# Performance work log

Hardware: AMD Instinct MI355X
Metric: run time of the kernel (lower is better)

## Reference

```python
import jax, jax.numpy as jnp
import numpy as np

MARGIN = 0.3
NEG_INF = jnp.float32(-1e30)


def setup_inputs() -> dict:
    key = jax.random.key(0)
    k1, k2 = jax.random.split(key)
    features = jax.random.normal(k1, (8192, 128), dtype=jnp.float32)
    labels = jax.random.randint(k2, (8192,), 0, 512)
    return {"features": features, "labels": labels}


def reference(features, labels):
    n = features.shape[0]
    # pairwise Euclidean distance, clamped like the torch code
    x2 = jnp.sum(features * features, axis=1, keepdims=True)          # [N,1]
    d2 = x2 + x2.T - 2.0 * (features @ features.T)                    # [N,N]
    dist = jnp.sqrt(jnp.clip(d2, 1e-8))

    same = labels[None, :] == labels[:, None]                          # [N,N]
    eye = jnp.eye(n, dtype=bool)
    pos_mask = same & ~eye                                             # positives, self excluded
    neg_mask = ~same

    # soft mining: softmax-weighted positive distance (weights ~ softmax(d))
    pos_logits = jnp.where(pos_mask, dist, NEG_INF)
    pw = jax.nn.softmax(pos_logits, axis=1)
    wp = jnp.sum(pw * jnp.where(pos_mask, dist, 0.0), axis=1)          # [N]

    # softmax-weighted negative distance (weights ~ softmax(-d))
    neg_logits = jnp.where(neg_mask, -dist, NEG_INF)
    nw = jax.nn.softmax(neg_logits, axis=1)
    wn = jnp.sum(nw * jnp.where(neg_mask, dist, 0.0), axis=1)          # [N]

    # soft margin: softplus(diff + margin)
    loss = jax.nn.softplus(wp - wn + MARGIN)

    # rows without any positive or any negative are skipped in the original
    valid = pos_mask.any(axis=1) & neg_mask.any(axis=1)
    loss = jnp.where(valid, loss, 0.0)
    denom = jnp.maximum(jnp.sum(valid.astype(jnp.float32)), 1.0)
    return jnp.sum(loss) / denom
```

## Files before the change

kernel.cpp:

```cpp
#include <hip/hip_runtime.h>
#include <hip/hip_bf16.h>


typedef __bf16 bf16x8 __attribute__((ext_vector_type(8)));
typedef float f32x4 __attribute__((ext_vector_type(4)));

#define NROWS 8192
#define DIM 128
#define JTILE 32
#define LDS_STRIDE 136
#define NLABELS 512
#define GCAP 64
#define JSPLIT 16
#define JSPAN (NROWS / JSPLIT)
#define JITERS (JSPAN / JTILE)
#define MARGIN_F 0.3f
#define AK1F 2.04027892f
#define AK1SQ 4.16273807f
#define EPS_T 2.08137e-8f
#define C2F (-43.2808512f)
#define LN2F 0.69314718f

__global__ __launch_bounds__(256) void prep_kernel(const float* __restrict__ F,
                                                   __hip_bfloat16* __restrict__ Fb,
                                                   float* __restrict__ x2,
                                                   float* __restrict__ gstat) {
    const int tid = threadIdx.x;
    const int wave = tid >> 6, lane = tid & 63;
    const int row = blockIdx.x * 4 + wave;
    float2 f = ((const float2*)(F + (size_t)row * DIM))[lane];
    f.x *= AK1F; f.y *= AK1F;
    ((__hip_bfloat162*)(Fb + (size_t)row * DIM))[lane] = __float22bfloat162_rn(f);
    float ss = f.x * f.x + f.y * f.y;
#pragma unroll
    for (int m = 32; m > 0; m >>= 1) ss += __shfl_xor(ss, m, 64);
    if (lane == 0) x2[row] = ss;
    if (blockIdx.x == 0 && tid < 4) gstat[tid] = 0.f;
}

template<bool DIAG>
__device__ __forceinline__ void tile_body(const __hip_bfloat16* __restrict__ sB,
                                          const float* __restrict__ sX2h,
                                          const bf16x8 (&a)[4],
                                          const float (&x2ih)[4],
                                          float (&nl4)[4], float (&ns4)[4],
                                          int lm, int quad, int ig0, int jbase) {
#pragma unroll
    for (int jt = 0; jt < 2; ++jt) {
        const int jl = jt * 16 + lm;
        const __hip_bfloat16* bp = sB + jl * LDS_STRIDE + quad * 8;
        const float xjh = sX2h[jl];
        f32x4 acc;
#pragma unroll
        for (int r = 0; r < 4; ++r) acc[r] = x2ih[r] + xjh;
#pragma unroll
        for (int kc = 0; kc < 4; ++kc) {
            bf16x8 b = *(const bf16x8*)(bp + kc * 32);
            acc = __builtin_amdgcn_mfma_f32_16x16x32_bf16(a[kc], b, acc, 0, 0, 0);
        }
        const int dj = jbase + jl - ig0;
#pragma unroll
        for (int r = 0; r < 4; ++r) {
            float d2h = fmaxf(-acc[r], EPS_T);
            float t = __builtin_amdgcn_sqrtf(d2h);
            float ne = __builtin_amdgcn_exp2f(-t);
            if (DIAG) ne = (dj == r) ? 0.f : ne;
            nl4[r] += ne;
            ns4[r] = fmaf(ne, t, ns4[r]);
        }
    }
}

__global__ __launch_bounds__(256, 3) void pairs_kernel(
        const __hip_bfloat16* __restrict__ Fb,
        const float* __restrict__ x2,
        const float* __restrict__ F,
        const int* __restrict__ labels,
        float2* __restrict__ partial,
        float4* __restrict__ corr) {
    __shared__ __hip_bfloat16 sB[2][JTILE * LDS_STRIDE];
    __shared__ float sX2[2][JTILE];
    __shared__ int sIdx[GCAP];
    __shared__ int sCnt;

    const int tid = threadIdx.x;
    const int bx = blockIdx.x, by = blockIdx.y;

    if (by < 4) {
        const int L = by * 128 + bx;
        if (tid == 0) sCnt = 0;
        __syncthreads();
        for (int it = 0; it < NROWS / 1024; ++it) {
            const int g = it * 1024 + tid * 4;
            int4 lv = *(const int4*)(labels + g);
#pragma unroll
            for (int k = 0; k < 4; ++k) {
                int lab = (k == 0) ? lv.x : (k == 1) ? lv.y : (k == 2) ? lv.z : lv.w;
                if (lab == L) {
                    int pos = atomicAdd(&sCnt, 1);
                    if (pos < GCAP) sIdx[pos] = g + k;
                }
            }
        }
        __syncthreads();
        const int gsz = sCnt < GCAP ? sCnt : GCAP;
        if (gsz > 0) {
            float* sAcc = (float*)sB;
            float* plA = sAcc;
            float* psA = sAcc + GCAP;
            float* nlA = sAcc + 2 * GCAP;
            float* nsA = sAcc + 3 * GCAP;
            if (tid < GCAP) { plA[tid] = 0.f; psA[tid] = 0.f; nlA[tid] = 0.f; nsA[tid] = 0.f; }
            __syncthreads();
            const int npair = gsz * gsz;
            for (int p = tid; p < npair; p += 256) {
                const int aI = p / gsz, bI = p - aI * gsz;
                if (aI == bI) continue;
                const float4* pa = (const float4*)(F + (size_t)sIdx[aI] * DIM);
                const float4* pb = (const float4*)(F + (size_t)sIdx[bI] * DIM);
                float dot = 0.f, ssa = 0.f, ssb = 0.f;
#pragma unroll 8
                for (int u = 0; u < 32; ++u) {
                    float4 va = pa[u], vb = pb[u];
                    dot = fmaf(va.x, vb.x, fmaf(va.y, vb.y, fmaf(va.z, vb.z, fmaf(va.w, vb.w, dot))));
                    ssa = fmaf(va.x, va.x, fmaf(va.y, va.y, fmaf(va.z, va.z, fmaf(va.w, va.w, ssa))));
                    ssb = fmaf(vb.x, vb.x, fmaf(vb.y, vb.y, fmaf(vb.z, vb.z, fmaf(vb.w, vb.w, ssb))));
                }
                float d2h = fmaxf((0.5f * (ssa + ssb) - dot) * AK1SQ, EPS_T);
                float t = __builtin_amdgcn_sqrtf(d2h);
                float ne = __builtin_amdgcn_exp2f(-t);
                float pe = __builtin_amdgcn_exp2f(t + C2F);
                unsafeAtomicAdd(&nlA[aI], ne);
                unsafeAtomicAdd(&nsA[aI], ne * t);
                unsafeAtomicAdd(&plA[aI], pe);
                unsafeAtomicAdd(&psA[aI], pe * t);
            }
            __syncthreads();
            if (tid < gsz)
                corr[sIdx[tid]] = make_float4(plA[tid], psA[tid], -nlA[tid], -nsA[tid]);
        }
        __syncthreads();
    }

    const int wave = tid >> 6;
    const int lane = tid & 63;
    const int quad = lane >> 4;
    const int lm = lane & 15;
    const int rbase = bx * 64 + wave * 16;

    bf16x8 a[4];
#pragma unroll
    for (int kc = 0; kc < 4; ++kc)
        a[kc] = *(const bf16x8*)(Fb + (size_t)(rbase + lm) * DIM + kc * 32 + quad * 8);

    const int ig0 = rbase + quad * 4;
    float x2ih[4];
#pragma unroll
    for (int r = 0; r < 4; ++r) x2ih[r] = -0.5f * x2[ig0 + r];

    float nl4[4] = {0,0,0,0}, ns4[4] = {0,0,0,0};

    const int j0 = by * JSPAN;
    const int djb0 = 2 * bx - by * JITERS;

    const int c0 = tid, c1 = tid + 256;
    uint4 st0, st1;
    float xv;
#define LOADTILE(JB) do {                                                      \
        const size_t jo = (size_t)(JB);                                        \
        st0 = *(const uint4*)(Fb + (jo + (c0 >> 4)) * DIM + (c0 & 15) * 8);    \
        st1 = *(const uint4*)(Fb + (jo + (c1 >> 4)) * DIM + (c1 & 15) * 8);    \
        if (tid < JTILE) xv = x2[jo + tid];                                    \
    } while (0)
#define WRITETILE(B) do {                                                      \
        __hip_bfloat16* sb = sB[B];                                            \
        *(uint4*)(sb + (c0 >> 4) * LDS_STRIDE + (c0 & 15) * 8) = st0;          \
        *(uint4*)(sb + (c1 >> 4) * LDS_STRIDE + (c1 & 15) * 8) = st1;          \
        if (tid < JTILE) sX2[B][tid] = -0.5f * xv;                             \
    } while (0)

    LOADTILE(j0);
    WRITETILE(0);
    __syncthreads();
    int cur = 0;
    for (int jb = 0; jb < JITERS; ++jb) {
        if (jb + 1 < JITERS) LOADTILE(j0 + (jb + 1) * JTILE);
        const int jbase = j0 + jb * JTILE;
        if ((unsigned)(jb - djb0) <= 1u)
            tile_body<true >(sB[cur], sX2[cur], a, x2ih, nl4, ns4, lm, quad, ig0, jbase);
        else
            tile_body<false>(sB[cur], sX2[cur], a, x2ih, nl4, ns4, lm, quad, ig0, jbase);
        if (jb + 1 < JITERS) WRITETILE(cur ^ 1);
        __syncthreads();
        cur ^= 1;
    }
#undef LOADTILE
#undef WRITETILE

#pragma unroll
    for (int m = 1; m < 16; m <<= 1) {
#pragma unroll
        for (int r = 0; r < 4; ++r) {
            nl4[r] += __shfl_xor(nl4[r], m, 64);
            ns4[r] += __shfl_xor(ns4[r], m, 64);
        }
    }
    if (lm == 0) {
#pragma unroll
        for (int r = 0; r < 4; ++r)
            partial[(size_t)by * NROWS + ig0 + r] = make_float2(nl4[r], ns4[r]);
    }
}

__global__ __launch_bounds__(256) void finalize_kernel(const float2* __restrict__ partial,
                                                       const float4* __restrict__ corr,
                                                       float* __restrict__ gstat,
                                                       float* __restrict__ out) {
    const int row = blockIdx.x * 256 + threadIdx.x;
    float4 c = corr[row];
    float nl = c.z, ns = c.w;
#pragma unroll
    for (int s = 0; s < JSPLIT; ++s) {
        float2 p = partial[(size_t)s * NROWS + row];
        nl += p.x; ns += p.y;
    }
    float sum = 0.f, cnt = 0.f;
    if (c.x > 0.f && nl > 0.f) {
        float x = fmaf(LN2F, c.y / c.x - ns / nl, MARGIN_F);
        sum = fmaxf(x, 0.f) + log1pf(__expf(-fabsf(x)));
        cnt = 1.f;
    }
#pragma unroll
    for (int m = 32; m > 0; m >>= 1) {
        sum += __shfl_xor(sum, m, 64);
        cnt += __shfl_xor(cnt, m, 64);
    }
    __shared__ float sS[4], sC[4];
    const int wave = threadIdx.x >> 6, lane = threadIdx.x & 63;
    if (lane == 0) { sS[wave] = sum; sC[wave] = cnt; }
    __syncthreads();
    if (threadIdx.x == 0) {
        unsafeAtomicAdd(&gstat[0], sS[0] + sS[1] + sS[2] + sS[3]);
        unsafeAtomicAdd(&gstat[1], sC[0] + sC[1] + sC[2] + sC[3]);
        __threadfence();
        unsigned t = atomicAdd((unsigned*)(gstat + 2), 1u);
        if (t == (unsigned)(gridDim.x - 1)) {
            float s2 = unsafeAtomicAdd(&gstat[0], 0.f);
            float c2 = unsafeAtomicAdd(&gstat[1], 0.f);
            out[0] = s2 / fmaxf(c2, 1.f);
        }
    }
}

extern "C" void kernel_launch(void* const* d_in, const int* in_sizes, int n_in,
                              void* d_out, int out_size, void* d_ws, size_t ws_size,
                              hipStream_t stream) {
    const float* F = (const float*)d_in[0];
    const int* labels = (const int*)d_in[1];
    float* out = (float*)d_out;

    char* ws = (char*)d_ws;
    __hip_bfloat16* Fb = (__hip_bfloat16*)ws;
    size_t off = (size_t)NROWS * DIM * 2;
    float* x2 = (float*)(ws + off);    off += (size_t)NROWS * 4;
    float4* corr = (float4*)(ws + off); off += (size_t)NROWS * 16;
    float2* partial = (float2*)(ws + off);
    off += (size_t)JSPLIT * NROWS * 8;
    float* gstat = (float*)(ws + off);

    prep_kernel<<<NROWS / 4, 256, 0, stream>>>(F, Fb, x2, gstat);
    pairs_kernel<<<dim3(NROWS / 64, JSPLIT), 256, 0, stream>>>(
        Fb, x2, F, labels, partial, corr);
    finalize_kernel<<<NROWS / 256, 256, 0, stream>>>(partial, corr, gstat, out);
}
```

Before: 109.7 us.

## Exploit distance symmetry: compute upper-triangle tiles and scatter column sums atomically

```diff
diff --git a/kernel.cpp b/kernel.cpp
--- a/kernel.cpp
+++ b/kernel.cpp
@@ -7,13 +7,12 @@
 
 #define NROWS 8192
 #define DIM 128
-#define JTILE 32
 #define LDS_STRIDE 136
 #define NLABELS 512
 #define GCAP 64
-#define JSPLIT 16
-#define JSPAN (NROWS / JSPLIT)
-#define JITERS (JSPAN / JTILE)
+#define NPAIR 64
+#define NCHUNK 32
+#define MTILES 129
 #define MARGIN_F 0.3f
 #define AK1F 2.04027892f
 #define AK1SQ 4.16273807f
@@ -44,9 +43,10 @@
                                           const bf16x8 (&a)[4],
                                           const float (&x2ih)[4],
                                           float (&nl4)[4], float (&ns4)[4],
+                                          float2* __restrict__ sColW,
                                           int lm, int quad, int ig0, int jbase) {
 #pragma unroll
-    for (int jt = 0; jt < 2; ++jt) {
+    for (int jt = 0; jt < 4; ++jt) {
         const int jl = jt * 16 + lm;
         const __hip_bfloat16* bp = sB + jl * LDS_STRIDE + quad * 8;
         const float xjh = sX2h[jl];
@@ -59,6 +59,7 @@
             acc = __builtin_amdgcn_mfma_f32_16x16x32_bf16(a[kc], b, acc, 0, 0, 0);
         }
         const int dj = jbase + jl - ig0;
+        float cl = 0.f, cs = 0.f;
 #pragma unroll
         for (int r = 0; r < 4; ++r) {
             float d2h = fmaxf(-acc[r], EPS_T);
@@ -67,6 +68,12 @@
             if (DIAG) ne = (dj == r) ? 0.f : ne;
             nl4[r] += ne;
             ns4[r] = fmaf(ne, t, ns4[r]);
+            if (!DIAG) { cl += ne; cs = fmaf(ne, t, cs); }
+        }
+        if (!DIAG) {
+            cl += __shfl_xor(cl, 16, 64); cl += __shfl_xor(cl, 32, 64);
+            cs += __shfl_xor(cs, 16, 64); cs += __shfl_xor(cs, 32, 64);
+            if (quad == 0) sColW[jl] = make_float2(cl, cs);
         }
     }
 }
@@ -76,18 +83,20 @@
         const float* __restrict__ x2,
         const float* __restrict__ F,
         const int* __restrict__ labels,
-        float2* __restrict__ partial,
+        float* __restrict__ accg,
         float4* __restrict__ corr) {
-    __shared__ __hip_bfloat16 sB[2][JTILE * LDS_STRIDE];
-    __shared__ float sX2[2][JTILE];
+    __shared__ __hip_bfloat16 sB[64 * LDS_STRIDE];
+    __shared__ float sX2[64];
+    __shared__ float2 sCol[4][64];
     __shared__ int sIdx[GCAP];
     __shared__ int sCnt;
 
     const int tid = threadIdx.x;
-    const int bx = blockIdx.x, by = blockIdx.y;
-
-    if (by < 4) {
-        const int L = by * 128 + bx;
+    const int p = blockIdx.x;
+    const int s = blockIdx.y;
+
+    if (s < 8) {
+        const int L = s * 64 + p;
         if (tid == 0) sCnt = 0;
         __syncthreads();
         for (int it = 0; it < NROWS / 1024; ++it) {
@@ -113,8 +122,8 @@
             if (tid < GCAP) { plA[tid] = 0.f; psA[tid] = 0.f; nlA[tid] = 0.f; nsA[tid] = 0.f; }
             __syncthreads();
             const int npair = gsz * gsz;
-            for (int p = tid; p < npair; p += 256) {
-                const int aI = p / gsz, bI = p - aI * gsz;
+            for (int pp = tid; pp < npair; pp += 256) {
+                const int aI = pp / gsz, bI = pp - aI * gsz;
                 if (aI == bI) continue;
                 const float4* pa = (const float4*)(F + (size_t)sIdx[aI] * DIM);
                 const float4* pb = (const float4*)(F + (size_t)sIdx[bI] * DIM);
@@ -146,84 +155,98 @@
     const int lane = tid & 63;
     const int quad = lane >> 4;
     const int lm = lane & 15;
-    const int rbase = bx * 64 + wave * 16;
-
-    bf16x8 a[4];
-#pragma unroll
-    for (int kc = 0; kc < 4; ++kc)
-        a[kc] = *(const bf16x8*)(Fb + (size_t)(rbase + lm) * DIM + kc * 32 + quad * 8);
-
-    const int ig0 = rbase + quad * 4;
-    float x2ih[4];
-#pragma unroll
-    for (int r = 0; r < 4; ++r) x2ih[r] = -0.5f * x2[ig0 + r];
-
-    float nl4[4] = {0,0,0,0}, ns4[4] = {0,0,0,0};
-
-    const int j0 = by * JSPAN;
-    const int djb0 = 2 * bx - by * JITERS;
-
-    const int c0 = tid, c1 = tid + 256;
-    uint4 st0, st1;
-    float xv;
-#define LOADTILE(JB) do {                                                      \
-        const size_t jo = (size_t)(JB);                                        \
-        st0 = *(const uint4*)(Fb + (jo + (c0 >> 4)) * DIM + (c0 & 15) * 8);    \
-        st1 = *(const uint4*)(Fb + (jo + (c1 >> 4)) * DIM + (c1 & 15) * 8);    \
-        if (tid < JTILE) xv = x2[jo + tid];                                    \
-    } while (0)
-#define WRITETILE(B) do {                                                      \
-        __hip_bfloat16* sb = sB[B];                                            \
-        *(uint4*)(sb + (c0 >> 4) * LDS_STRIDE + (c0 & 15) * 8) = st0;          \
-        *(uint4*)(sb + (c1 >> 4) * LDS_STRIDE + (c1 & 15) * 8) = st1;          \
-        if (tid < JTILE) sX2[B][tid] = -0.5f * xv;                             \
-    } while (0)
-
-    LOADTILE(j0);
-    WRITETILE(0);
-    __syncthreads();
-    int cur = 0;
-    for (int jb = 0; jb < JITERS; ++jb) {
-        if (jb + 1 < JITERS) LOADTILE(j0 + (jb + 1) * JTILE);
-        const int jbase = j0 + jb * JTILE;
-        if ((unsigned)(jb - djb0) <= 1u)
-            tile_body<true >(sB[cur], sX2[cur], a, x2ih, nl4, ns4, lm, quad, ig0, jbase);
-        else
-            tile_body<false>(sB[cur], sX2[cur], a, x2ih, nl4, ns4, lm, quad, ig0, jbase);
-        if (jb + 1 < JITERS) WRITETILE(cur ^ 1);
-        __syncthreads();
-        cur ^= 1;
-    }
-#undef LOADTILE
-#undef WRITETILE
-
-#pragma unroll
-    for (int m = 1; m < 16; m <<= 1) {
-#pragma unroll
-        for (int r = 0; r < 4; ++r) {
-            nl4[r] += __shfl_xor(nl4[r], m, 64);
-            ns4[r] += __shfl_xor(ns4[r], m, 64);
-        }
-    }
-    if (lm == 0) {
-#pragma unroll
-        for (int r = 0; r < 4; ++r)
-            partial[(size_t)by * NROWS + ig0 + r] = make_float2(nl4[r], ns4[r]);
-    }
-}
-
-__global__ __launch_bounds__(256) void finalize_kernel(const float2* __restrict__ partial,
+
+    const int nA = 128 - p;
+    const int tlo = (s * MTILES) >> 5;
+    const int thi = ((s + 1) * MTILES) >> 5;
+
+#pragma unroll 1
+    for (int phase = 0; phase < 2; ++phase) {
+        const int a = (phase == 0) ? p : 127 - p;
+        const int t0 = (phase == 0) ? tlo : (tlo > nA ? tlo : nA);
+        const int t1 = (phase == 0) ? (thi < nA ? thi : nA) : thi;
+        if (t0 >= t1) continue;
+
+        const int rbase = a * 64 + wave * 16;
+        bf16x8 afr[4];
+#pragma unroll
+        for (int kc = 0; kc < 4; ++kc)
+            afr[kc] = *(const bf16x8*)(Fb + (size_t)(rbase + lm) * DIM + kc * 32 + quad * 8);
+        const int ig0 = rbase + quad * 4;
+        float x2ih[4];
+#pragma unroll
+        for (int r = 0; r < 4; ++r) x2ih[r] = -0.5f * x2[ig0 + r];
+        float nl4[4] = {0,0,0,0}, ns4[4] = {0,0,0,0};
+
+        int prevj = -1;
+        for (int t = t0; t < t1; ++t) {
+            const int jb = (phase == 0) ? (p + t) : (127 - p) + (t - nA);
+            const int jbase = jb << 6;
+            __syncthreads();
+            if (prevj >= 0 && tid < 64) {
+                float2 c0 = sCol[0][tid], c1 = sCol[1][tid];
+                float2 c2 = sCol[2][tid], c3 = sCol[3][tid];
+                unsafeAtomicAdd(accg + (size_t)(prevj + tid) * 2,
+                                c0.x + c1.x + c2.x + c3.x);
+                unsafeAtomicAdd(accg + (size_t)(prevj + tid) * 2 + 1,
+                                c0.y + c1.y + c2.y + c3.y);
+            }
+#pragma unroll
+            for (int s2 = 0; s2 < 4; ++s2) {
+                int c = tid + s2 * 256;
+                int jr = c >> 4, ck = c & 15;
+                *(bf16x8*)(sB + jr * LDS_STRIDE + ck * 8) =
+                    *(const bf16x8*)(Fb + (size_t)(jbase + jr) * DIM + ck * 8);
+            }
+            if (tid < 64) sX2[tid] = -0.5f * x2[jbase + tid];
+            __syncthreads();
+
+            if (jb == a) {
+                tile_body<true >(sB, sX2, afr, x2ih, nl4, ns4, sCol[wave],
+                                 lm, quad, ig0, jbase);
+                prevj = -1;
+            } else {
+                tile_body<false>(sB, sX2, afr, x2ih, nl4, ns4, sCol[wave],
+                                 lm, quad, ig0, jbase);
+                prevj = jbase;
+            }
+        }
+
+#pragma unroll
+        for (int m = 1; m < 16; m <<= 1) {
+#pragma unroll
+            for (int r = 0; r < 4; ++r) {
+                nl4[r] += __shfl_xor(nl4[r], m, 64);
+                ns4[r] += __shfl_xor(ns4[r], m, 64);
+            }
+        }
+        if (lm == 0) {
+#pragma unroll
+            for (int r = 0; r < 4; ++r) {
+                unsafeAtomicAdd(accg + (size_t)(ig0 + r) * 2, nl4[r]);
+                unsafeAtomicAdd(accg + (size_t)(ig0 + r) * 2 + 1, ns4[r]);
+            }
+        }
+        __syncthreads();
+        if (prevj >= 0 && tid < 64) {
+            float2 c0 = sCol[0][tid], c1 = sCol[1][tid];
+            float2 c2 = sCol[2][tid], c3 = sCol[3][tid];
+            unsafeAtomicAdd(accg + (size_t)(prevj + tid) * 2,
+                            c0.x + c1.x + c2.x + c3.x);
+            unsafeAtomicAdd(accg + (size_t)(prevj + tid) * 2 + 1,
+                            c0.y + c1.y + c2.y + c3.y);
+        }
+    }
+}
+
+__global__ __launch_bounds__(256) void finalize_kernel(const float* __restrict__ accg,
                                                        const float4* __restrict__ corr,
                                                        float* __restrict__ gstat,
                                                        float* __restrict__ out) {
     const int row = blockIdx.x * 256 + threadIdx.x;
     float4 c = corr[row];
-    float nl = c.z, ns = c.w;
-#pragma unroll
-    for (int s = 0; s < JSPLIT; ++s) {
-        float2 p = partial[(size_t)s * NROWS + row];
-        nl += p.x; ns += p.y;
-    }
+    float nl = c.z + accg[(size_t)row * 2];
+    float ns = c.w + accg[(size_t)row * 2 + 1];
     float sum = 0.f, cnt = 0.f;
     if (c.x > 0.f && nl > 0.f) {
         float x = fmaf(LN2F, c.y / c.x - ns / nl, MARGIN_F);
@@ -264,12 +287,12 @@
     size_t off = (size_t)NROWS * DIM * 2;
     float* x2 = (float*)(ws + off);    off += (size_t)NROWS * 4;
     float4* corr = (float4*)(ws + off); off += (size_t)NROWS * 16;
-    float2* partial = (float2*)(ws + off);
-    off += (size_t)JSPLIT * NROWS * 8;
+    float* accg = (float*)(ws + off);  off += (size_t)NROWS * 8;
     float* gstat = (float*)(ws + off);
 
+    hipMemsetAsync(accg, 0, (size_t)NROWS * 8, stream);
     prep_kernel<<<NROWS / 4, 256, 0, stream>>>(F, Fb, x2, gstat);
-    pairs_kernel<<<dim3(NROWS / 64, JSPLIT), 256, 0, stream>>>(
-        Fb, x2, F, labels, partial, corr);
-    finalize_kernel<<<NROWS / 256, 256, 0, stream>>>(partial, corr, gstat, out);
-}
+    pairs_kernel<<<dim3(NPAIR, NCHUNK), 256, 0, stream>>>(
+        Fb, x2, F, labels, accg, corr);
+    finalize_kernel<<<NROWS / 256, 256, 0, stream>>>(accg, corr, gstat, out);
+}
```

New measurement: 116.0 us. 1.06x slower.

## Build label groups in prep kernel and compute intra-group corrections from bf16

Applied to the files above, without the earlier changes.

```diff
diff --git a/kernel.cpp b/kernel.cpp
--- a/kernel.cpp
+++ b/kernel.cpp
@@ -16,15 +16,16 @@
 #define JITERS (JSPAN / JTILE)
 #define MARGIN_F 0.3f
 #define AK1F 2.04027892f
-#define AK1SQ 4.16273807f
 #define EPS_T 2.08137e-8f
 #define C2F (-43.2808512f)
 #define LN2F 0.69314718f
 
 __global__ __launch_bounds__(256) void prep_kernel(const float* __restrict__ F,
+                                                   const int* __restrict__ labels,
                                                    __hip_bfloat16* __restrict__ Fb,
                                                    float* __restrict__ x2,
-                                                   float* __restrict__ gstat) {
+                                                   int* __restrict__ gcnt,
+                                                   int* __restrict__ gslot) {
     const int tid = threadIdx.x;
     const int wave = tid >> 6, lane = tid & 63;
     const int row = blockIdx.x * 4 + wave;
@@ -34,8 +35,12 @@
     float ss = f.x * f.x + f.y * f.y;
 #pragma unroll
     for (int m = 32; m > 0; m >>= 1) ss += __shfl_xor(ss, m, 64);
-    if (lane == 0) x2[row] = ss;
-    if (blockIdx.x == 0 && tid < 4) gstat[tid] = 0.f;
+    if (lane == 0) {
+        x2[row] = ss;
+        const int lab = labels[row];
+        int pos = atomicAdd(&gcnt[lab], 1);
+        if (pos < GCAP) gslot[lab * GCAP + pos] = row;
+    }
 }
 
 template<bool DIAG>
@@ -74,36 +79,20 @@
 __global__ __launch_bounds__(256, 3) void pairs_kernel(
         const __hip_bfloat16* __restrict__ Fb,
         const float* __restrict__ x2,
-        const float* __restrict__ F,
-        const int* __restrict__ labels,
+        const int* __restrict__ gcnt,
+        const int* __restrict__ gslot,
         float2* __restrict__ partial,
         float4* __restrict__ corr) {
     __shared__ __hip_bfloat16 sB[2][JTILE * LDS_STRIDE];
     __shared__ float sX2[2][JTILE];
-    __shared__ int sIdx[GCAP];
-    __shared__ int sCnt;
 
     const int tid = threadIdx.x;
     const int bx = blockIdx.x, by = blockIdx.y;
 
     if (by < 4) {
         const int L = by * 128 + bx;
-        if (tid == 0) sCnt = 0;
-        __syncthreads();
-        for (int it = 0; it < NROWS / 1024; ++it) {
-            const int g = it * 1024 + tid * 4;
-            int4 lv = *(const int4*)(labels + g);
-#pragma unroll
-            for (int k = 0; k < 4; ++k) {
-                int lab = (k == 0) ? lv.x : (k == 1) ? lv.y : (k == 2) ? lv.z : lv.w;
-                if (lab == L) {
-                    int pos = atomicAdd(&sCnt, 1);
-                    if (pos < GCAP) sIdx[pos] = g + k;
-                }
-            }
-        }
-        __syncthreads();
-        const int gsz = sCnt < GCAP ? sCnt : GCAP;
+        const int cnt = gcnt[L];
+        const int gsz = cnt < GCAP ? cnt : GCAP;
         if (gsz > 0) {
             float* sAcc = (float*)sB;
             float* plA = sAcc;
@@ -116,17 +105,19 @@
             for (int p = tid; p < npair; p += 256) {
                 const int aI = p / gsz, bI = p - aI * gsz;
                 if (aI == bI) continue;
-                const float4* pa = (const float4*)(F + (size_t)sIdx[aI] * DIM);
-                const float4* pb = (const float4*)(F + (size_t)sIdx[bI] * DIM);
-                float dot = 0.f, ssa = 0.f, ssb = 0.f;
-#pragma unroll 8
-                for (int u = 0; u < 32; ++u) {
-                    float4 va = pa[u], vb = pb[u];
-                    dot = fmaf(va.x, vb.x, fmaf(va.y, vb.y, fmaf(va.z, vb.z, fmaf(va.w, vb.w, dot))));
-                    ssa = fmaf(va.x, va.x, fmaf(va.y, va.y, fmaf(va.z, va.z, fmaf(va.w, va.w, ssa))));
-                    ssb = fmaf(vb.x, vb.x, fmaf(vb.y, vb.y, fmaf(vb.z, vb.z, fmaf(vb.w, vb.w, ssb))));
+                const int ia = gslot[L * GCAP + aI];
+                const int ib = gslot[L * GCAP + bI];
+                const bf16x8* pa = (const bf16x8*)(Fb + (size_t)ia * DIM);
+                const bf16x8* pb = (const bf16x8*)(Fb + (size_t)ib * DIM);
+                float dot = 0.f;
+#pragma unroll 4
+                for (int u = 0; u < 16; ++u) {
+                    bf16x8 va = pa[u], vb = pb[u];
+#pragma unroll
+                    for (int e = 0; e < 8; ++e)
+                        dot = fmaf((float)va[e], (float)vb[e], dot);
                 }
-                float d2h = fmaxf((0.5f * (ssa + ssb) - dot) * AK1SQ, EPS_T);
+                float d2h = fmaxf(0.5f * (x2[ia] + x2[ib]) - dot, EPS_T);
                 float t = __builtin_amdgcn_sqrtf(d2h);
                 float ne = __builtin_amdgcn_exp2f(-t);
                 float pe = __builtin_amdgcn_exp2f(t + C2F);
@@ -137,7 +128,8 @@
             }
             __syncthreads();
             if (tid < gsz)
-                corr[sIdx[tid]] = make_float4(plA[tid], psA[tid], -nlA[tid], -nsA[tid]);
+                corr[gslot[L * GCAP + tid]] =
+                    make_float4(plA[tid], psA[tid], -nlA[tid], -nsA[tid]);
         }
         __syncthreads();
     }
@@ -264,12 +256,14 @@
     size_t off = (size_t)NROWS * DIM * 2;
     float* x2 = (float*)(ws + off);    off += (size_t)NROWS * 4;
     float4* corr = (float4*)(ws + off); off += (size_t)NROWS * 16;
+    int* gcnt = (int*)(ws + off);      off += (size_t)NLABELS * 4;
+    float* gstat = (float*)(ws + off); off += 16;
+    int* gslot = (int*)(ws + off);     off += (size_t)NLABELS * GCAP * 4;
     float2* partial = (float2*)(ws + off);
-    off += (size_t)JSPLIT * NROWS * 8;
-    float* gstat = (float*)(ws + off);
-
-    prep_kernel<<<NROWS / 4, 256, 0, stream>>>(F, Fb, x2, gstat);
+
+    hipMemsetAsync(gcnt, 0, (size_t)NLABELS * 4 + 16, stream);
+    prep_kernel<<<NROWS / 4, 256, 0, stream>>>(F, labels, Fb, x2, gcnt, gslot);
     pairs_kernel<<<dim3(NROWS / 64, JSPLIT), 256, 0, stream>>>(
-        Fb, x2, F, labels, partial, corr);
+        Fb, x2, gcnt, gslot, partial, corr);
     finalize_kernel<<<NROWS / 256, 256, 0, stream>>>(partial, corr, gstat, out);
 }
```

New measurement: 113.7 us. +3.7%, slower.
